# Kernel tuning notes

Hardware: AMD Instinct MI355X
Metric: run time of the kernel (lower is better)

## Reference

```python
import jax, jax.numpy as jnp
import numpy as np

EMBED = 2048
NUM_HEADS = 16
N_KV_HEADS = 4
HEAD_DIM = EMBED // NUM_HEADS  # 128
MAX_SEQ = 2048
BATCH = 4


def _sincos_pos_emb(dim, max_seq_len):
    position = np.arange(max_seq_len, dtype=np.float32)[:, None]
    div_term = np.exp(np.arange(0, dim, 2, dtype=np.float32) * (-np.log(10000.0) / dim))
    pe = np.zeros((max_seq_len, dim), dtype=np.float32)
    pe[:, 0::2] = np.sin(position * div_term)
    pe[:, 1::2] = np.cos(position * div_term)
    return jnp.asarray(pe)


def setup_inputs() -> dict:
    key = jax.random.key(0)
    ks = jax.random.split(key, 7)
    s_in = 1.0 / np.sqrt(EMBED)
    kv_dim = N_KV_HEADS * HEAD_DIM
    return {
        "x": jax.random.normal(ks[0], (BATCH, MAX_SEQ, EMBED), dtype=jnp.float32),
        "wq_w": jax.random.normal(ks[1], (EMBED, EMBED), dtype=jnp.float32) * s_in,
        "wq_b": jax.random.normal(ks[2], (EMBED,), dtype=jnp.float32) * 0.01,
        "wk_w": jax.random.normal(ks[3], (EMBED, kv_dim), dtype=jnp.float32) * s_in,
        "wk_b": jax.random.normal(ks[4], (kv_dim,), dtype=jnp.float32) * 0.01,
        "wv_w": jax.random.normal(ks[5], (EMBED, kv_dim), dtype=jnp.float32) * s_in,
        "wv_b": jax.random.normal(ks[6], (kv_dim,), dtype=jnp.float32) * 0.01,
        "pos_emb": _sincos_pos_emb(EMBED, MAX_SEQ),
    }


def reference(x, wq_w, wq_b, wk_w, wk_b, wv_w, wv_b, pos_emb):
    b, s, e = x.shape
    H, Hkv, d = NUM_HEADS, N_KV_HEADS, HEAD_DIM
    rep = H // Hkv
    scale = 1.0 / float(np.sqrt(d))

    # projections + additive sincos positional embedding on Q and K
    xq = (x @ wq_w + wq_b).reshape(b, s, H, d) + pos_emb[:s].reshape(1, s, H, d)
    xk = (x @ wk_w + wk_b).reshape(b, s, Hkv, d) \
        + pos_emb[:s, : Hkv * d].reshape(1, s, Hkv, d)
    xv = (x @ wv_w + wv_b).reshape(b, s, Hkv, d)

    # GQA: group query heads per kv head instead of materializing repeat_kv
    xqg = xq.reshape(b, s, Hkv, rep, d)  # [b, q, kv_heads, rep, d]
    scores = jnp.einsum('bqkrd,bskd->bkrqs', xqg, xk) * scale  # [b,kv,rep,q,s]
    probs = jax.nn.softmax(scores.astype(jnp.float32), axis=-1)
    out = jnp.einsum('bkrqs,bskd->bqkrd', probs, xv.astype(jnp.float32))
    return out.reshape(b, s, e)
```

## Files before the change

kernel.cpp:

```cpp
#include <hip/hip_runtime.h>
#include <hip/hip_bf16.h>
#include <cstdint>

#define B_   4
#define S_   2048
#define E_   2048
#define H_   16
#define HKV_ 4
#define D_   128
#define KVD_ 512
#define NQKV 3072
#define QSCALE 0.1275253129f

typedef __bf16 bf16x8_t __attribute__((ext_vector_type(8)));
typedef float  f32x4_t  __attribute__((ext_vector_type(4)));
typedef float  f32x16_t __attribute__((ext_vector_type(16)));

__device__ __forceinline__ ushort f2bf(float f) {
  uint32_t u = __builtin_bit_cast(uint32_t, f);
  uint32_t r = u + 0x7FFFu + ((u >> 16) & 1u);
  return (ushort)(r >> 16);
}

__device__ __forceinline__ void gload16(const void* g, void* l) {
  __builtin_amdgcn_global_load_lds(
      (__attribute__((address_space(1))) void*)g,
      (__attribute__((address_space(3))) void*)l, 16, 0, 0);
}

__device__ __forceinline__ uint32_t cvtpk(float lo, float hi) {
  uint32_t r;
  asm volatile("v_cvt_pk_bf16_f32 %0, %1, %2" : "=v"(r) : "v"(lo), "v"(hi));
  return r;
}

__device__ __forceinline__ void plswap(uint32_t& a, uint32_t& b) {
  asm volatile("v_permlane32_swap_b32 %0, %1" : "+v"(a), "+v"(b));
}

__global__ __launch_bounds__(256) void k_cvt_x(const float* __restrict__ x,
                                               ushort* __restrict__ xb) {
  int i = blockIdx.x * 256 + threadIdx.x;
  const float4* p = (const float4*)x + (size_t)i * 2;
  float4 a = p[0], b = p[1];
  uint4 o;
  o.x = (uint32_t)f2bf(a.x) | ((uint32_t)f2bf(a.y) << 16);
  o.y = (uint32_t)f2bf(a.z) | ((uint32_t)f2bf(a.w) << 16);
  o.z = (uint32_t)f2bf(b.x) | ((uint32_t)f2bf(b.y) << 16);
  o.w = (uint32_t)f2bf(b.z) | ((uint32_t)f2bf(b.w) << 16);
  ((uint4*)xb)[i] = o;
}

__global__ __launch_bounds__(256) void k_cvt_w_t(const float* __restrict__ w,
                                                 ushort* __restrict__ wb,
                                                 int C, int n_off) {
  __shared__ ushort t[32][33];
  int c0 = blockIdx.x * 32, r0 = blockIdx.y * 32;
  int tx = threadIdx.x, ty = threadIdx.y;
#pragma unroll
  for (int i = 0; i < 4; ++i) {
    int r = ty + i * 8;
    t[r][tx] = f2bf(w[(size_t)(r0 + r) * C + c0 + tx]);
  }
  __syncthreads();
#pragma unroll
  for (int i = 0; i < 4; ++i) {
    int c = ty + i * 8;
    wb[(size_t)(n_off + c0 + c) * E_ + r0 + tx] = t[tx][c];
  }
}

__global__ __launch_bounds__(256) void k_gemm(
    const ushort* __restrict__ xb, const ushort* __restrict__ wb,
    const float* __restrict__ wq_b, const float* __restrict__ wk_b,
    const float* __restrict__ wv_b, const float* __restrict__ pos,
    ushort* __restrict__ qkv) {
  __shared__ ushort As[128 * 64];
  __shared__ ushort Bs[128 * 64];
  int tid = threadIdx.x;
  int wid = tid >> 6, lane = tid & 63;
  int l15 = lane & 15, l4 = lane >> 4;
  int wr = wid >> 1, wc = wid & 1;
  int m0 = blockIdx.y * 128, n0 = blockIdx.x * 128;
  f32x4_t acc[4][4] = {};

  for (int k0 = 0; k0 < E_; k0 += 64) {
#pragma unroll
    for (int it = 0; it < 4; ++it) {
      int p = it * 256 + tid;
      int row = p >> 3, c = p & 7;
      gload16(xb + (size_t)(m0 + row) * E_ + k0 + c * 8,
              (char*)As + (size_t)(it * 256 + wid * 64) * 16);
      gload16(wb + (size_t)(n0 + row) * E_ + k0 + c * 8,
              (char*)Bs + (size_t)(it * 256 + wid * 64) * 16);
    }
    __syncthreads();
#pragma unroll
    for (int kk = 0; kk < 2; ++kk) {
      bf16x8_t a[4], b[4];
#pragma unroll
      for (int mi = 0; mi < 4; ++mi)
        a[mi] = *(const bf16x8_t*)&As[(wr * 64 + mi * 16 + l15) * 64 + kk * 32 + l4 * 8];
#pragma unroll
      for (int ni = 0; ni < 4; ++ni)
        b[ni] = *(const bf16x8_t*)&Bs[(wc * 64 + ni * 16 + l15) * 64 + kk * 32 + l4 * 8];
#pragma unroll
      for (int mi = 0; mi < 4; ++mi)
#pragma unroll
        for (int ni = 0; ni < 4; ++ni)
          acc[mi][ni] = __builtin_amdgcn_mfma_f32_16x16x32_bf16(
              a[mi], b[ni], acc[mi][ni], 0, 0, 0);
    }
    __syncthreads();
  }
#pragma unroll
  for (int mi = 0; mi < 4; ++mi) {
#pragma unroll
    for (int ni = 0; ni < 4; ++ni) {
      int n = n0 + wc * 64 + ni * 16 + l15;
      int mbase = m0 + wr * 64 + mi * 16 + l4 * 4;
#pragma unroll
      for (int r = 0; r < 4; ++r) {
        int m = mbase + r;
        int srow = m & (S_ - 1);
        float v = acc[mi][ni][r];
        if (n < E_)
          v = (v + wq_b[n] + pos[(size_t)srow * E_ + n]) * QSCALE;
        else if (n < E_ + KVD_)
          v = v + wk_b[n - E_] + pos[(size_t)srow * E_ + (n - E_)];
        else
          v = v + wv_b[n - E_ - KVD_];
        qkv[(size_t)m * NQKV + n] = f2bf(v);
      }
    }
  }
}

__global__ __launch_bounds__(256) void k_v_t(const ushort* __restrict__ qkv,
                                             ushort* __restrict__ vt) {
  __shared__ ushort t[32][33];
  int b = blockIdx.z >> 2, kh = blockIdx.z & 3;
  int s0 = blockIdx.x * 32, d0 = blockIdx.y * 32;
  int tx = threadIdx.x, ty = threadIdx.y;
#pragma unroll
  for (int i = 0; i < 4; ++i) {
    int s = s0 + ty + i * 8;
    t[ty + i * 8][tx] =
        qkv[(size_t)(b * S_ + s) * NQKV + E_ + KVD_ + kh * D_ + d0 + tx];
  }
  __syncthreads();
#pragma unroll
  for (int i = 0; i < 4; ++i) {
    int d = d0 + ty + i * 8;
    vt[(size_t)((b * HKV_ + kh) * D_ + d) * S_ + s0 + tx] = t[tx][ty + i * 8];
  }
}

__global__ __launch_bounds__(512, 2) void k_attn(const ushort* __restrict__ qkv,
                                                 const ushort* __restrict__ vt,
                                                 float* __restrict__ out) {
  __shared__ char lds[2][32768];
  int tid = threadIdx.x, wid = tid >> 6, lane = tid & 63;
  int l31 = lane & 31, hi = lane >> 5;
  int bh = blockIdx.y;
  int b = bh >> 4, h = bh & 15, kh = h >> 2;
  int qw0 = blockIdx.x * 256 + wid * 32;

  bf16x8_t qf[8];
  {
    const ushort* qg = qkv + (size_t)(b * S_ + qw0 + l31) * NQKV + h * D_ + hi * 8;
#pragma unroll
    for (int k = 0; k < 8; ++k) qf[k] = *(const bf16x8_t*)(qg + k * 16);
  }

  const ushort* kbase = qkv + (size_t)b * S_ * NQKV + E_ + kh * D_;
  const ushort* vbase = vt + (size_t)(b * HKV_ + kh) * D_ * S_;

  int rk0 = wid * 4 + (lane >> 4);
  int dk0 = ((lane & 15) * 8);
  int dv0 = wid * 8 + (lane >> 3);
  int kv0 = ((lane & 7) * 8);

  f32x16_t ao[4] = {};
  float mrow = -1e30f, lsum = 0.f;

#define STAGE(key0, bufp)                                                      \
  {                                                                            \
    char* bp_ = (bufp);                                                        \
    _Pragma("unroll")                                                          \
    for (int i = 0; i < 2; ++i) {                                              \
      int rk = i * 32 + rk0;                                                   \
      int dk = dk0 ^ ((rk & 7) << 3);                                          \
      gload16(kbase + (size_t)((key0) + rk) * NQKV + dk,                       \
              bp_ + i * 8192 + wid * 1024);                                    \
      int dv = i * 64 + dv0;                                                   \
      int kv = kv0 ^ ((dv & 7) << 3);                                          \
      gload16(vbase + (size_t)dv * S_ + (key0) + kv,                           \
              bp_ + 16384 + i * 8192 + wid * 1024);                            \
    }                                                                          \
  }

  STAGE(0, lds[0]);
  __syncthreads();

  int cur = 0;
  const int nt = S_ / 64;
  for (int t = 0; t < nt; ++t) {
    if (t + 1 < nt) STAGE((t + 1) * 64, lds[cur ^ 1]);

    const ushort* Ks = (const ushort*)(lds[cur]);
    const ushort* Vs = (const ushort*)(lds[cur] + 16384);

    f32x16_t sc[2] = {};
#pragma unroll
    for (int kb = 0; kb < 2; ++kb) {
      int row = kb * 32 + l31;
      const ushort* kr = Ks + row * 128;
      int sw = (l31 & 7) << 3;
#pragma unroll
      for (int ks = 0; ks < 8; ++ks) {
        bf16x8_t kf = *(const bf16x8_t*)(kr + ((ks * 16 + hi * 8) ^ sw));
        sc[kb] = __builtin_amdgcn_mfma_f32_32x32x16_bf16(kf, qf[ks], sc[kb], 0, 0, 0);
      }
    }

    float tmax = sc[0][0];
#pragma unroll
    for (int r = 1; r < 16; ++r) tmax = fmaxf(tmax, sc[0][r]);
#pragma unroll
    for (int r = 0; r < 16; ++r) tmax = fmaxf(tmax, sc[1][r]);
    tmax = fmaxf(tmax, __shfl_xor(tmax, 32));

    if (!__all(tmax - mrow <= 8.f)) {
      float mnew = fmaxf(mrow, tmax);
      float f = __builtin_amdgcn_exp2f(mrow - mnew);
      mrow = mnew;
      lsum *= f;
#pragma unroll
      for (int r = 0; r < 16; ++r) {
        float fr = __shfl(f, (r & 3) + 8 * (r >> 2) + 4 * hi);
        ao[0][r] *= fr; ao[1][r] *= fr; ao[2][r] *= fr; ao[3][r] *= fr;
      }
    }

    float rs = 0.f;
#pragma unroll
    for (int kb = 0; kb < 2; ++kb)
#pragma unroll
      for (int r = 0; r < 16; ++r) {
        float p = __builtin_amdgcn_exp2f(sc[kb][r] - mrow);
        sc[kb][r] = p;
        rs += p;
      }
    rs += __shfl_xor(rs, 32);
    lsum += rs;

    bf16x8_t pa[4];
#pragma unroll
    for (int kb = 0; kb < 2; ++kb) {
      uint32_t c0 = cvtpk(sc[kb][0], sc[kb][1]);
      uint32_t c1 = cvtpk(sc[kb][2], sc[kb][3]);
      uint32_t c2 = cvtpk(sc[kb][4], sc[kb][5]);
      uint32_t c3 = cvtpk(sc[kb][6], sc[kb][7]);
      uint32_t c4 = cvtpk(sc[kb][8], sc[kb][9]);
      uint32_t c5 = cvtpk(sc[kb][10], sc[kb][11]);
      uint32_t c6 = cvtpk(sc[kb][12], sc[kb][13]);
      uint32_t c7 = cvtpk(sc[kb][14], sc[kb][15]);
      plswap(c0, c2); plswap(c1, c3); plswap(c4, c6); plswap(c5, c7);
      uint4 u0 = {c0, c1, c2, c3};
      uint4 u1 = {c4, c5, c6, c7};
      pa[kb * 2]     = __builtin_bit_cast(bf16x8_t, u0);
      pa[kb * 2 + 1] = __builtin_bit_cast(bf16x8_t, u1);
    }

#pragma unroll
    for (int dblk = 0; dblk < 4; ++dblk) {
      int row = dblk * 32 + l31;
      const ushort* vr = Vs + row * 64;
      int sw = (l31 & 7) << 3;
#pragma unroll
      for (int ks = 0; ks < 4; ++ks) {
        bf16x8_t vf = *(const bf16x8_t*)(vr + ((ks * 16 + hi * 8) ^ sw));
        ao[dblk] = __builtin_amdgcn_mfma_f32_32x32x16_bf16(pa[ks], vf, ao[dblk], 0, 0, 0);
      }
    }

    __syncthreads();
    cur ^= 1;
  }

  float rinv = 1.0f / lsum;
#pragma unroll
  for (int r = 0; r < 16; ++r) {
    float rv = __shfl(rinv, (r & 3) + 8 * (r >> 2) + 4 * hi);
    int q = qw0 + (r & 3) + 8 * (r >> 2) + 4 * hi;
    float* og = out + (size_t)(b * S_ + q) * E_ + h * D_ + l31;
#pragma unroll
    for (int dblk = 0; dblk < 4; ++dblk)
      og[dblk * 32] = ao[dblk][r] * rv;
  }
#undef STAGE
}

extern "C" void kernel_launch(void* const* d_in, const int* in_sizes, int n_in,
                              void* d_out, int out_size, void* d_ws, size_t ws_size,
                              hipStream_t stream) {
  const float* x    = (const float*)d_in[0];
  const float* wq_w = (const float*)d_in[1];
  const float* wq_b = (const float*)d_in[2];
  const float* wk_w = (const float*)d_in[3];
  const float* wk_b = (const float*)d_in[4];
  const float* wv_w = (const float*)d_in[5];
  const float* wv_b = (const float*)d_in[6];
  const float* pos  = (const float*)d_in[7];
  float* out = (float*)d_out;

  ushort* xb  = (ushort*)d_out;
  ushort* wb  = (ushort*)((char*)d_out + 33554432);
  ushort* qkv = (ushort*)d_ws;
  ushort* vt  = (ushort*)((char*)d_ws + 50331648);

  k_cvt_x<<<dim3((B_ * S_ * E_) / 8 / 256), 256, 0, stream>>>(x, xb);
  dim3 tb(32, 8);
  k_cvt_w_t<<<dim3(E_ / 32, E_ / 32), tb, 0, stream>>>(wq_w, wb, E_, 0);
  k_cvt_w_t<<<dim3(KVD_ / 32, E_ / 32), tb, 0, stream>>>(wk_w, wb, KVD_, E_);
  k_cvt_w_t<<<dim3(KVD_ / 32, E_ / 32), tb, 0, stream>>>(wv_w, wb, KVD_, E_ + KVD_);
  k_gemm<<<dim3(NQKV / 128, (B_ * S_) / 128), 256, 0, stream>>>(
      xb, wb, wq_b, wk_b, wv_b, pos, qkv);
  k_v_t<<<dim3(S_ / 32, D_ / 32, B_ * HKV_), tb, 0, stream>>>(qkv, vt);
  k_attn<<<dim3(S_ / 256, B_ * H_), 512, 0, stream>>>(qkv, vt, out);
}
```

Baseline: 486.0 us.

## Rewrite QKV GEMM as 256x256-tile double-buffered pipeline with swizzled LDS

Replaces the 128x128 single-buffered QKV projection GEMM with a 256x256 tile per 512-thread block. Global loads for the next K tiles are issued between quadrant MFMA phases into a double-buffered 128KB LDS region with an XOR swizzle, using explicit vmcnt/lgkmcnt waits and barriers. It also remaps block IDs for L2 locality and raises MFMA issue priority. The aim is to hide load latency and cut LDS bank conflicts, at the cost of heavy LDS use, high register pressure and fragile hand-tuned wait counts.

```diff
diff --git a/kernel.cpp b/kernel.cpp
--- a/kernel.cpp
+++ b/kernel.cpp
@@ -70,70 +70,143 @@
   }
 }
 
-__global__ __launch_bounds__(256) void k_gemm(
+__global__ __launch_bounds__(512, 2) void k_gemm(
     const ushort* __restrict__ xb, const ushort* __restrict__ wb,
     const float* __restrict__ wq_b, const float* __restrict__ wk_b,
     const float* __restrict__ wv_b, const float* __restrict__ pos,
     ushort* __restrict__ qkv) {
-  __shared__ ushort As[128 * 64];
-  __shared__ ushort Bs[128 * 64];
-  int tid = threadIdx.x;
-  int wid = tid >> 6, lane = tid & 63;
+  __shared__ char ldsb[131072];
+  int tid = threadIdx.x, wid = tid >> 6, lane = tid & 63;
   int l15 = lane & 15, l4 = lane >> 4;
-  int wr = wid >> 1, wc = wid & 1;
-  int m0 = blockIdx.y * 128, n0 = blockIdx.x * 128;
-  f32x4_t acc[4][4] = {};
-
-  for (int k0 = 0; k0 < E_; k0 += 64) {
-#pragma unroll
-    for (int it = 0; it < 4; ++it) {
-      int p = it * 256 + tid;
-      int row = p >> 3, c = p & 7;
-      gload16(xb + (size_t)(m0 + row) * E_ + k0 + c * 8,
-              (char*)As + (size_t)(it * 256 + wid * 64) * 16);
-      gload16(wb + (size_t)(n0 + row) * E_ + k0 + c * 8,
-              (char*)Bs + (size_t)(it * 256 + wid * 64) * 16);
-    }
-    __syncthreads();
-#pragma unroll
-    for (int kk = 0; kk < 2; ++kk) {
-      bf16x8_t a[4], b[4];
-#pragma unroll
-      for (int mi = 0; mi < 4; ++mi)
-        a[mi] = *(const bf16x8_t*)&As[(wr * 64 + mi * 16 + l15) * 64 + kk * 32 + l4 * 8];
-#pragma unroll
-      for (int ni = 0; ni < 4; ++ni)
-        b[ni] = *(const bf16x8_t*)&Bs[(wc * 64 + ni * 16 + l15) * 64 + kk * 32 + l4 * 8];
-#pragma unroll
-      for (int mi = 0; mi < 4; ++mi)
-#pragma unroll
-        for (int ni = 0; ni < 4; ++ni)
-          acc[mi][ni] = __builtin_amdgcn_mfma_f32_16x16x32_bf16(
-              a[mi], b[ni], acc[mi][ni], 0, 0, 0);
-    }
-    __syncthreads();
-  }
-#pragma unroll
-  for (int mi = 0; mi < 4; ++mi) {
-#pragma unroll
-    for (int ni = 0; ni < 4; ++ni) {
-      int n = n0 + wc * 64 + ni * 16 + l15;
-      int mbase = m0 + wr * 64 + mi * 16 + l4 * 4;
-#pragma unroll
-      for (int r = 0; r < 4; ++r) {
-        int m = mbase + r;
-        int srow = m & (S_ - 1);
-        float v = acc[mi][ni][r];
-        if (n < E_)
-          v = (v + wq_b[n] + pos[(size_t)srow * E_ + n]) * QSCALE;
-        else if (n < E_ + KVD_)
-          v = v + wk_b[n - E_] + pos[(size_t)srow * E_ + (n - E_)];
-        else
-          v = v + wv_b[n - E_ - KVD_];
-        qkv[(size_t)m * NQKV + n] = f2bf(v);
-      }
-    }
-  }
+  int wm = wid >> 2, wn = wid & 3;
+
+  int bid = blockIdx.x;
+  bid = (bid & 7) * 48 + (bid >> 3);
+  int tm = bid & 31, tn = bid >> 5;
+  int m0 = tm * 256, n0 = tn * 256;
+
+#define STAGE_A(TILE, MH)                                                      \
+  {                                                                            \
+    char* sb_ = ldsb + (((TILE)&1) * 32768) + ((MH) * 16384);                  \
+    _Pragma("unroll") for (int i_ = 0; i_ < 2; ++i_) {                         \
+      int s_ = i_ * 8 + wid;                                                   \
+      int r_ = s_ * 8 + (lane >> 3);                                           \
+      int cg_ = (lane & 7) ^ ((lane >> 3) & 7);                                \
+      gload16(xb + (size_t)(m0 + (MH) * 128 + r_) * E_ + (TILE) * 64 + cg_ * 8,\
+              sb_ + s_ * 1024);                                                \
+    }                                                                          \
+  }
+#define STAGE_B(TILE, NH)                                                      \
+  {                                                                            \
+    char* sb_ = ldsb + 65536 + (((TILE)&1) * 32768) + ((NH) * 16384);          \
+    _Pragma("unroll") for (int i_ = 0; i_ < 2; ++i_) {                         \
+      int s_ = i_ * 8 + wid;                                                   \
+      int r_ = s_ * 8 + (lane >> 3);                                           \
+      int cg_ = (lane & 7) ^ ((lane >> 3) & 7);                                \
+      gload16(wb + (size_t)(n0 + (NH) * 128 + r_) * E_ + (TILE) * 64 + cg_ * 8,\
+              sb_ + s_ * 1024);                                                \
+    }                                                                          \
+  }
+#define READ_A(DST, SLOT)                                                      \
+  _Pragma("unroll") for (int mi_ = 0; mi_ < 4; ++mi_)                          \
+  _Pragma("unroll") for (int kk_ = 0; kk_ < 2; ++kk_) {                        \
+    int r_ = wm * 64 + mi_ * 16 + l15;                                         \
+    int c_ = (kk_ * 4 + l4) ^ (r_ & 7);                                        \
+    DST[mi_][kk_] = *(const bf16x8_t*)((SLOT) + r_ * 128 + c_ * 16);           \
+  }
+#define READ_B(DST, SLOT)                                                      \
+  _Pragma("unroll") for (int ni_ = 0; ni_ < 2; ++ni_)                          \
+  _Pragma("unroll") for (int kk_ = 0; kk_ < 2; ++kk_) {                        \
+    int r_ = wn * 32 + ni_ * 16 + l15;                                         \
+    int c_ = (kk_ * 4 + l4) ^ (r_ & 7);                                        \
+    DST[ni_][kk_] = *(const bf16x8_t*)((SLOT) + r_ * 128 + c_ * 16);           \
+  }
+#define MFMA_QUAD(MH, NH, AF, BF)                                              \
+  __builtin_amdgcn_s_setprio(1);                                               \
+  _Pragma("unroll") for (int kk_ = 0; kk_ < 2; ++kk_)                          \
+  _Pragma("unroll") for (int mi_ = 0; mi_ < 4; ++mi_)                          \
+  _Pragma("unroll") for (int ni_ = 0; ni_ < 2; ++ni_)                          \
+    acc[(MH) * 4 + mi_][(NH) * 2 + ni_] =                                      \
+        __builtin_amdgcn_mfma_f32_16x16x32_bf16(                               \
+            AF[mi_][kk_], BF[ni_][kk_], acc[(MH) * 4 + mi_][(NH) * 2 + ni_],   \
+            0, 0, 0);                                                          \
+  __builtin_amdgcn_s_setprio(0);
+#define LGKM0()                                                                \
+  asm volatile("s_waitcnt lgkmcnt(0)" ::: "memory");                           \
+  __builtin_amdgcn_sched_barrier(0);
+#define BAR() __builtin_amdgcn_s_barrier();
+
+  f32x4_t acc[8][4] = {};
+
+  const int NT = E_ / 64;
+  STAGE_A(0, 0); STAGE_B(0, 0); STAGE_A(0, 1); STAGE_B(0, 1);
+  STAGE_A(1, 0); STAGE_B(1, 0);
+  asm volatile("s_waitcnt vmcnt(8)" ::: "memory");
+  BAR();
+
+  for (int t = 0; t < NT; ++t) {
+    const char* Ab = ldsb + (t & 1) * 32768;
+    const char* Bb = ldsb + 65536 + (t & 1) * 32768;
+    bf16x8_t af[4][2], b0[2][2], b1[2][2];
+
+    READ_A(af, Ab);
+    READ_B(b0, Bb);
+    if (t + 1 < NT) STAGE_A(t + 1, 1);
+    BAR(); LGKM0();
+    MFMA_QUAD(0, 0, af, b0);
+    asm volatile("s_waitcnt vmcnt(6)" ::: "memory");
+    BAR();
+
+    READ_B(b1, Bb + 16384);
+    if (t + 1 < NT) STAGE_B(t + 1, 1);
+    BAR(); LGKM0();
+    MFMA_QUAD(0, 1, af, b1);
+    BAR();
+
+    READ_A(af, Ab + 16384);
+    if (t + 2 < NT) STAGE_A(t + 2, 0);
+    BAR(); LGKM0();
+    MFMA_QUAD(1, 0, af, b0);
+    BAR();
+
+    if (t + 2 < NT) STAGE_B(t + 2, 0);
+    BAR();
+    MFMA_QUAD(1, 1, af, b1);
+    asm volatile("s_waitcnt vmcnt(8)" ::: "memory");
+    BAR();
+  }
+
+#pragma unroll
+  for (int mh = 0; mh < 2; ++mh)
+#pragma unroll
+    for (int mi = 0; mi < 4; ++mi)
+#pragma unroll
+      for (int nh = 0; nh < 2; ++nh)
+#pragma unroll
+        for (int ni = 0; ni < 2; ++ni) {
+          int n = n0 + nh * 128 + wn * 32 + ni * 16 + l15;
+          int mbase = m0 + mh * 128 + wm * 64 + mi * 16 + l4 * 4;
+#pragma unroll
+          for (int r = 0; r < 4; ++r) {
+            int m = mbase + r;
+            int srow = m & (S_ - 1);
+            float v = acc[mh * 4 + mi][nh * 2 + ni][r];
+            if (n < E_)
+              v = (v + wq_b[n] + pos[(size_t)srow * E_ + n]) * QSCALE;
+            else if (n < E_ + KVD_)
+              v = v + wk_b[n - E_] + pos[(size_t)srow * E_ + (n - E_)];
+            else
+              v = v + wv_b[n - E_ - KVD_];
+            qkv[(size_t)m * NQKV + n] = f2bf(v);
+          }
+        }
+#undef STAGE_A
+#undef STAGE_B
+#undef READ_A
+#undef READ_B
+#undef MFMA_QUAD
+#undef LGKM0
+#undef BAR
 }
 
 __global__ __launch_bounds__(256) void k_v_t(const ushort* __restrict__ qkv,
@@ -325,8 +398,7 @@
   k_cvt_w_t<<<dim3(E_ / 32, E_ / 32), tb, 0, stream>>>(wq_w, wb, E_, 0);
   k_cvt_w_t<<<dim3(KVD_ / 32, E_ / 32), tb, 0, stream>>>(wk_w, wb, KVD_, E_);
   k_cvt_w_t<<<dim3(KVD_ / 32, E_ / 32), tb, 0, stream>>>(wv_w, wb, KVD_, E_ + KVD_);
-  k_gemm<<<dim3(NQKV / 128, (B_ * S_) / 128), 256, 0, stream>>>(
-      xb, wb, wq_b, wk_b, wv_b, pos, qkv);
+  k_gemm<<<dim3(384), 512, 0, stream>>>(xb, wb, wq_b, wk_b, wv_b, pos, qkv);
   k_v_t<<<dim3(S_ / 32, D_ / 32, B_ * HKV_), tb, 0, stream>>>(qkv, vt);
   k_attn<<<dim3(S_ / 256, B_ * H_), 512, 0, stream>>>(qkv, vt, out);
 }
```

After: 485.8 us. No clear change (-0.1%).
